# Kernel optimization log

Measured on AMD Instinct MI355X. Metric: run time of the kernel, lower is better.

## Reference

```python
import jax, jax.numpy as jnp
import numpy as np

# 27 kernel taps x 3 offset components (dz, dy, dx), matching the module's offset0 list.
OFFSET0 = np.array([
    1, 1, 1, 1, 1, 0, 1, 1, -1, 1, 0, 1, 1, 0, 0, 1, 0, -1, 1, -1, 1, 1, -1, 0, 1, -1, -1,
    0, 1, 1, 0, 1, 0, 0, 1, -1, 0, 0, 1, 0, 0, 0, 0, 0, -1, 0, -1, 1, 0, -1, 0, 0, -1, -1,
    -1, 1, 1, -1, 1, 0, -1, 1, -1, -1, 0, 1, -1, 0, 0, -1, 0, -1, -1, -1, 1, -1, -1, 0, -1, -1, -1
], dtype=np.float64).reshape(27, 3)

BN_EPS = 1e-5


def upsample_nearest2(x):
    # nn.Upsample(scale_factor=2), default mode='nearest', on [B,C,Z,Y,X]
    x = jnp.repeat(x, 2, axis=2)
    x = jnp.repeat(x, 2, axis=3)
    return jnp.repeat(x, 2, axis=4)


def deform_conv3d_static(x, W, b, alpha):
    """3D deformable conv, kernel 3, pad 1, stride 1, with spatially-constant
    per-tap offsets alpha*OFFSET0. Zero padding outside; trilinear sampling.
    Since offsets are static, each tap samples at a fixed fractional shift,
    implemented as a static trilinear combination of slices of the padded input.
    x: [B,C,Z,Y,X], W: [O,C,3,3,3], b: [O].
    """
    B, C, Z, Y, X = x.shape
    # pad 2: 1 for the 3x3x3 kernel + 1 for fractional offsets (|alpha*d| <= 0.7)
    xp = jnp.pad(x, ((0, 0), (0, 0), (2, 2), (2, 2), (2, 2)))
    out = None
    t = 0
    for kz in range(3):
        for ky in range(3):
            for kx in range(3):
                dz, dy, dx = (alpha * OFFSET0[t]).tolist()
                s = (kz - 1 + dz, ky - 1 + dy, kx - 1 + dx)  # shift rel. to output voxel
                f = [int(np.floor(v)) for v in s]
                w = [v - fl for v, fl in zip(s, f)]
                vol = None
                for cz in (0, 1):
                    for cy in (0, 1):
                        for cx in (0, 1):
                            wt = ((w[0] if cz else 1.0 - w[0]) *
                                  (w[1] if cy else 1.0 - w[1]) *
                                  (w[2] if cx else 1.0 - w[2]))
                            if wt == 0.0:
                                continue
                            z0 = 2 + f[0] + cz
                            y0 = 2 + f[1] + cy
                            x0 = 2 + f[2] + cx
                            sl = xp[:, :, z0:z0 + Z, y0:y0 + Y, x0:x0 + X]
                            sl = jnp.float32(wt) * sl
                            vol = sl if vol is None else vol + sl
                contrib = jnp.einsum('oc,bczyx->bozyx', W[:, :, kz, ky, kx], vol)
                out = contrib if out is None else out + contrib
                t += 1
    return out + b[None, :, None, None, None]


def batchnorm(x, g, bt, m, v):
    # eval-mode BatchNorm3d over channel axis 1
    inv = g * jax.lax.rsqrt(v + BN_EPS)
    return x * inv[None, :, None, None, None] + (bt - m * inv)[None, :, None, None, None]


def setup_inputs() -> dict:
    key = jax.random.key(0)
    ks = jax.random.split(key, 13)
    ch_in, ch_out = 64, 32
    x = jax.random.normal(ks[0], (1, ch_in, 32, 32, 32), jnp.float32)
    w_def = jax.random.normal(ks[1], (ch_out, ch_in, 3, 3, 3), jnp.float32) * 0.05
    b_def = jax.random.normal(ks[2], (ch_out,), jnp.float32) * 0.05
    bn1_g = 1.0 + 0.1 * jax.random.normal(ks[3], (ch_out,), jnp.float32)
    bn1_b = 0.1 * jax.random.normal(ks[4], (ch_out,), jnp.float32)
    bn1_m = 0.1 * jax.random.normal(ks[5], (ch_out,), jnp.float32)
    bn1_v = jax.random.uniform(ks[6], (ch_out,), jnp.float32, 0.5, 1.5)
    w_comb = jax.random.normal(ks[7], (ch_out, 3 * ch_out), jnp.float32) * 0.1
    b_comb = 0.05 * jax.random.normal(ks[8], (ch_out,), jnp.float32)
    bn2_g = 1.0 + 0.1 * jax.random.normal(ks[9], (ch_out,), jnp.float32)
    bn2_b = 0.1 * jax.random.normal(ks[10], (ch_out,), jnp.float32)
    bn2_m = 0.1 * jax.random.normal(ks[11], (ch_out,), jnp.float32)
    bn2_v = jax.random.uniform(ks[12], (ch_out,), jnp.float32, 0.5, 1.5)
    return {"x": x, "w_def": w_def, "b_def": b_def,
            "bn1_g": bn1_g, "bn1_b": bn1_b, "bn1_m": bn1_m, "bn1_v": bn1_v,
            "w_comb": w_comb, "b_comb": b_comb,
            "bn2_g": bn2_g, "bn2_b": bn2_b, "bn2_m": bn2_m, "bn2_v": bn2_v}


def reference(x, w_def, b_def, bn1_g, bn1_b, bn1_m, bn1_v,
              w_comb, b_comb, bn2_g, bn2_b, bn2_m, bn2_v):
    xu = upsample_nearest2(x)
    branches = []
    for alpha in (0.0, 0.4, 0.7):  # shared deform-conv weights, three static offset scales
        o = deform_conv3d_static(xu, w_def, b_def, alpha)
        o = jax.nn.relu(batchnorm(o, bn1_g, bn1_b, bn1_m, bn1_v))
        branches.append(o)
    cat = jnp.concatenate(branches, axis=1)  # [B, 3*ch_out, Z,Y,X]
    y = jnp.einsum('oc,bczyx->bozyx', w_comb, cat) + b_comb[None, :, None, None, None]
    y = batchnorm(y, bn2_g, bn2_b, bn2_m, bn2_v)
    return jax.nn.relu(y)
```

## Files before the change

kernel.cpp:

```cpp
#include <hip/hip_runtime.h>


typedef __bf16 bf16x8 __attribute__((ext_vector_type(8)));
typedef float f32x16 __attribute__((ext_vector_type(16)));
typedef unsigned u32x2 __attribute__((ext_vector_type(2)));

__device__ inline unsigned short f2bf(float f) {
  unsigned int u = __float_as_uint(f);
  u += 0x7FFFu + ((u >> 16) & 1u);
  return (unsigned short)(u >> 16);
}

__device__ inline bf16x8 bc16(uint4 v) { return __builtin_bit_cast(bf16x8, v); }

__device__ inline unsigned cvtpk(float lo, float hi) {
  unsigned r;
  asm("v_cvt_pk_bf16_f32 %0, %1, %2" : "=v"(r) : "v"(lo), "v"(hi));
  return r;
}

__device__ inline void plswap(unsigned& a, unsigned& b) {
  u32x2 r = __builtin_amdgcn_permlane32_swap(a, b, false, false);
  a = r.x;
  b = r.y;
}

__device__ inline void gload16(const unsigned short* g, unsigned short* l) {
  __builtin_amdgcn_global_load_lds(
      (const __attribute__((address_space(1))) unsigned int*)(const void*)g,
      (__attribute__((address_space(3))) unsigned int*)(void*)l, 16, 0, 0);
}

__device__ inline float ucoef(int abit, int k, int jbit, float alpha) {
  if (abit == 0) return (k == 0) ? (jbit ? alpha : 1.f - alpha) : (jbit ? 1.f : 0.f);
  return (k == 2) ? (jbit ? 1.f - alpha : alpha) : (jbit ? 0.f : 1.f);
}

__global__ void k_prep(const float* __restrict__ x, unsigned short* __restrict__ xT,
                       const float* __restrict__ w_def, const float* __restrict__ bn1_g,
                       const float* __restrict__ bn1_v, unsigned short* __restrict__ W_sw,
                       const float* __restrict__ w_comb, const float* __restrict__ b_comb,
                       const float* __restrict__ bn2_g, const float* __restrict__ bn2_b,
                       const float* __restrict__ bn2_m, const float* __restrict__ bn2_v,
                       const float* __restrict__ b_def, const float* __restrict__ bn1_b,
                       const float* __restrict__ bn1_m, unsigned short* __restrict__ W2_sw,
                       float* __restrict__ bias1, float* __restrict__ bias2) {
  __shared__ unsigned short t[64][65];
  int bid = blockIdx.x;
  if (bid < 512) {
    int s0 = bid * 64;
    int lane = threadIdx.x & 63;
    int grp = threadIdx.x >> 6;
#pragma unroll
    for (int c = grp; c < 64; c += 4)
      t[c][lane] = f2bf(x[c * 32768 + s0 + lane]);
    __syncthreads();
#pragma unroll
    for (int s = grp; s < 64; s += 4)
      xT[(size_t)(s0 + s) * 64 + lane] = t[lane][s];
  } else if (bid < 2048) {
    int e = (bid - 512) * 256 + threadIdx.x;
    int j = e & 7;
    int lane = (e >> 3) & 63;
    int idx = e >> 9;
    int nt = idx % 3;
    idx /= 3;
    int s = idx & 31;
    int p = idx >> 5;
    int o = lane & 31;
    int br = nt;
    int kk = 16 * s + ((lane >> 5) << 3) + j;
    int tap = kk >> 6, ch = kk & 63;
    int jz = (tap >> 2) & 1, jy = (tap >> 1) & 1, jx = tap & 1;
    int a = (p >> 2) & 1, b = (p >> 1) & 1, cp = p & 1;
    float alpha = (br == 0) ? 0.f : ((br == 1) ? 0.4f : 0.7f);
    const float* wb = w_def + (o * 64 + ch) * 27;
    float sum = 0.f;
    for (int kz = 0; kz < 3; ++kz) {
      float uz = ucoef(a, kz, jz, alpha);
      if (uz == 0.f) continue;
      for (int ky = 0; ky < 3; ++ky) {
        float uy = ucoef(b, ky, jy, alpha);
        if (uy == 0.f) continue;
        float uzy = uz * uy;
        for (int kx = 0; kx < 3; ++kx) {
          float ux = ucoef(cp, kx, jx, alpha);
          if (ux != 0.f) sum += wb[kz * 9 + ky * 3 + kx] * uzy * ux;
        }
      }
    }
    float s1 = bn1_g[o] * rsqrtf(bn1_v[o] + 1e-5f);
    W_sw[e] = f2bf(sum * s1);
  } else {
    int tid = threadIdx.x;
    for (int e = tid; e < 3072; e += 256) {
      int j = e & 7;
      int lane = (e >> 3) & 63;
      int s2 = e >> 9;
      int n = lane & 31;
      int k = 16 * s2 + ((lane >> 5) << 3) + j;
      float sc2 = bn2_g[n] * rsqrtf(bn2_v[n] + 1e-5f);
      W2_sw[e] = f2bf(w_comb[n * 96 + k] * sc2);
    }
    if (tid < 32) {
      float s1 = bn1_g[tid] * rsqrtf(bn1_v[tid] + 1e-5f);
      bias1[tid] = (b_def[tid] - bn1_m[tid]) * s1 + bn1_b[tid];
      float s2 = bn2_g[tid] * rsqrtf(bn2_v[tid] + 1e-5f);
      bias2[tid] = (b_comb[tid] - bn2_m[tid]) * s2 + bn2_b[tid];
    }
  }
}

__launch_bounds__(512, 2)
__global__ void k_main(const unsigned short* __restrict__ xT,
                       const unsigned short* __restrict__ W_sw,
                       const unsigned short* __restrict__ W2_sw,
                       const float* __restrict__ bias1f,
                       const float* __restrict__ bias2f,
                       float* __restrict__ out) {
  __shared__ unsigned short xt[51840];
  __shared__ unsigned short wring[2][6144];
  __shared__ float blds[64];
  int tid = threadIdx.x;
  int lane = tid & 63;
  int wv = tid >> 6;
  int bid = blockIdx.x;
  int bph = bid & 1, a = (bid >> 1) & 1;
  int tb = bid >> 2;
  int tx = tb & 3, ty = (tb >> 2) & 3, tz = tb >> 4;
  int i0 = tz * 8, j0 = ty * 8, k0 = tx * 8;

  for (int t2 = tid; t2 < 6480; t2 += 512) {
    int cblk = t2 & 7;
    int r = t2 >> 3;
    int xrel = r % 10;
    int zy = r / 10;
    int yrel = zy % 9;
    int zrel = zy / 9;
    int gz = i0 + a - 1 + zrel, gy = j0 + bph - 1 + yrel, gx = k0 - 1 + xrel;
    uint4 v = make_uint4(0u, 0u, 0u, 0u);
    if ((unsigned)gz < 32u && (unsigned)gy < 32u && (unsigned)gx < 32u)
      v = *(const uint4*)(xT + ((((gz * 32 + gy) * 32 + gx) << 6) + (cblk << 3)));
    *(uint4*)(xt + ((r << 6) + (((cblk + r) << 3) & 63))) = v;
  }
  if (tid < 32) {
    blds[tid] = bias1f[tid];
    blds[32 + tid] = bias2f[tid];
  }

  bf16x8 b2f[6];
  const uint4* w2q = (const uint4*)W2_sw;
#pragma unroll
  for (int s2 = 0; s2 < 6; ++s2) b2f[s2] = bc16(w2q[s2 * 64 + lane]);
  __syncthreads();

  int h = lane >> 5, h8 = h << 3;
  int m = lane & 31;
  int ax = m & 7, ay = (m >> 3) & 1, az = m >> 4;
  int zs = wv >> 2, ys = wv & 3;
  int dz0 = 4 * zs + az;
  int dy = 2 * ys + ay;
  int p0 = (a << 2) | (bph << 1);

  auto stage = [&](int pn, int tn, int slot) {
    if (wv < 6) {
      const unsigned short* g =
          W_sw + (size_t)pn * 49152 + tn * 6144 + wv * 1024 + lane * 8;
      unsigned short* l = &wring[slot][wv * 1024];
      gload16(g, l);
      gload16(g + 512, l + 512);
    }
  };

  stage(p0, 0, 0);

  volatile const float* vbl = blds;
  f32x16 osv0, osv1;

#pragma unroll
  for (int cp = 0; cp < 2; ++cp) {
    f32x16 acc[2][3];
#pragma unroll
    for (int mt = 0; mt < 2; ++mt)
#pragma unroll
      for (int nt = 0; nt < 3; ++nt) acc[mt][nt] = (f32x16)0.f;

#pragma unroll
    for (int t = 0; t < 8; ++t) {
      int c = cp * 8 + t;
      asm volatile("s_waitcnt vmcnt(0)" ::: "memory");
      __builtin_amdgcn_s_barrier();
      __builtin_amdgcn_sched_barrier(0);
      if (c < 15) {
        int cn = c + 1;
        stage(p0 | (cn >> 3), cn & 7, cn & 1);
      }
      __builtin_amdgcn_sched_barrier(0);
      const unsigned short* wb = &wring[c & 1][0];
      int jz = (t >> 2) & 1, jy = (t >> 1) & 1, jx = t & 1;
      int row0 = ((dz0 + jz) * 9 + (dy + jy)) * 10 + (ax + cp + jx);
      int row1 = row0 + 180;
      __builtin_amdgcn_s_setprio(1);
#pragma unroll
      for (int q = 0; q < 4; ++q) {
        int c0 = (q << 4) + h8;
        int e0 = (row0 << 6) + ((c0 + (row0 << 3)) & 63);
        int e1 = (row1 << 6) + ((c0 + (row1 << 3)) & 63);
        bf16x8 a0 = bc16(*(const uint4*)(xt + e0));
        bf16x8 a1 = bc16(*(const uint4*)(xt + e1));
        const unsigned short* wf = wb + q * 1536 + lane * 8;
        bf16x8 bb0 = bc16(*(const uint4*)(wf));
        bf16x8 bb1 = bc16(*(const uint4*)(wf + 512));
        bf16x8 bb2 = bc16(*(const uint4*)(wf + 1024));
        acc[0][0] = __builtin_amdgcn_mfma_f32_32x32x16_bf16(bb0, a0, acc[0][0], 0, 0, 0);
        acc[1][0] = __builtin_amdgcn_mfma_f32_32x32x16_bf16(bb0, a1, acc[1][0], 0, 0, 0);
        acc[0][1] = __builtin_amdgcn_mfma_f32_32x32x16_bf16(bb1, a0, acc[0][1], 0, 0, 0);
        acc[1][1] = __builtin_amdgcn_mfma_f32_32x32x16_bf16(bb1, a1, acc[1][1], 0, 0, 0);
        acc[0][2] = __builtin_amdgcn_mfma_f32_32x32x16_bf16(bb2, a0, acc[0][2], 0, 0, 0);
        acc[1][2] = __builtin_amdgcn_mfma_f32_32x32x16_bf16(bb2, a1, acc[1][2], 0, 0, 0);
      }
      __builtin_amdgcn_s_setprio(0);
      __builtin_amdgcn_sched_barrier(0);
    }

#pragma unroll
    for (int mt = 0; mt < 2; ++mt) {
      uint4 fr[6];
#pragma unroll
      for (int nt = 0; nt < 3; ++nt) {
        unsigned ww[8];
#pragma unroll
        for (int qc = 0; qc < 8; ++qc) {
          int q = qc >> 1, c2 = qc & 1;
          int r0 = 4 * q + 2 * c2;
          int row = (r0 & 3) + ((r0 >> 2) << 3) + (h << 2);
          float lo = fmaxf(acc[mt][nt][r0] + vbl[row], 0.f);
          float hi = fmaxf(acc[mt][nt][r0 + 1] + vbl[row + 1], 0.f);
          ww[2 * q + c2] = cvtpk(lo, hi);
        }
        plswap(ww[0], ww[2]);
        plswap(ww[1], ww[3]);
        plswap(ww[4], ww[6]);
        plswap(ww[5], ww[7]);
        fr[2 * nt] = make_uint4(ww[0], ww[1], ww[2], ww[3]);
        fr[2 * nt + 1] = make_uint4(ww[4], ww[5], ww[6], ww[7]);
      }
      f32x16 acc2 = (f32x16)0.f;
#pragma unroll
      for (int s2 = 0; s2 < 6; ++s2)
        acc2 = __builtin_amdgcn_mfma_f32_32x32x16_bf16(b2f[s2], bc16(fr[s2]), acc2, 0, 0, 0);
      if (cp == 0) {
        f32x16 ov;
#pragma unroll
        for (int r = 0; r < 16; ++r) {
          int row = (r & 3) + ((r >> 2) << 3) + (h << 2);
          ov[r] = fmaxf(acc2[r] + vbl[32 + row], 0.f);
        }
        if (mt == 0) osv0 = ov; else osv1 = ov;
      } else {
        f32x16 prev = (mt == 0) ? osv0 : osv1;
        int Z = 2 * (i0 + 4 * zs + 2 * mt + az) + a;
        int Y = 2 * (j0 + dy) + bph;
        float2* o2 = (float2*)out;
#pragma unroll
        for (int r = 0; r < 16; ++r) {
          int ch = (r & 3) + ((r >> 2) << 3) + (h << 2);
          float v1 = fmaxf(acc2[r] + vbl[32 + ch], 0.f);
          o2[((size_t)ch << 17) + ((size_t)Z << 11) + (Y << 5) + (k0 + ax)] =
              make_float2(prev[r], v1);
        }
      }
    }
  }
}

extern "C" void kernel_launch(void* const* d_in, const int* in_sizes, int n_in,
                              void* d_out, int out_size, void* d_ws, size_t ws_size,
                              hipStream_t stream) {
  (void)in_sizes; (void)n_in; (void)out_size; (void)ws_size;
  const float* x      = (const float*)d_in[0];
  const float* w_def  = (const float*)d_in[1];
  const float* b_def  = (const float*)d_in[2];
  const float* bn1_g  = (const float*)d_in[3];
  const float* bn1_b  = (const float*)d_in[4];
  const float* bn1_m  = (const float*)d_in[5];
  const float* bn1_v  = (const float*)d_in[6];
  const float* w_comb = (const float*)d_in[7];
  const float* b_comb = (const float*)d_in[8];
  const float* bn2_g  = (const float*)d_in[9];
  const float* bn2_b  = (const float*)d_in[10];
  const float* bn2_m  = (const float*)d_in[11];
  const float* bn2_v  = (const float*)d_in[12];

  char* ws = (char*)d_ws;
  unsigned short* xT   = (unsigned short*)(ws);
  unsigned short* W_sw = (unsigned short*)(ws + 4194304);
  unsigned short* W2sw = (unsigned short*)(ws + 4980736);
  float* bias1 = (float*)(ws + 4986880);
  float* bias2 = (float*)(ws + 4987008);
  float* out = (float*)d_out;

  hipLaunchKernelGGL(k_prep, dim3(2049), dim3(256), 0, stream,
                     x, xT, w_def, bn1_g, bn1_v, W_sw,
                     w_comb, b_comb, bn2_g, bn2_b, bn2_m, bn2_v,
                     b_def, bn1_b, bn1_m, W2sw, bias1, bias2);
  hipLaunchKernelGGL(k_main, dim3(256), dim3(512), 0, stream,
                     xT, W_sw, W2sw, bias1, bias2, out);
}
```

Measured before the change: 62.77 us.

## Stage two weight taps per barrier and stagger per-wave quarter order

The weight ring slots double in size so each stage loads two taps (12288 elements) using all eight waves instead of six. That halves the number of barrier/wait stages from 16 to 8. Each wave now starts its inner loop at a different quarter offset (qr), which spreads LDS bank accesses across waves. The loop over stages is no longer fully unrolled, the epilogue for the first half runs conditionally inside the loop, and the volatile bias reads become plain LDS reads. The costs are more LDS per block, which could threaten two blocks per CU, and different code generation for the partly rolled loop.

Result: faster. 52.91 us (-15.7%).

```diff
diff --git a/kernel.cpp b/kernel.cpp
--- a/kernel.cpp
+++ b/kernel.cpp
@@ -119,7 +119,7 @@
                        const float* __restrict__ bias2f,
                        float* __restrict__ out) {
   __shared__ unsigned short xt[51840];
-  __shared__ unsigned short wring[2][6144];
+  __shared__ unsigned short wring[2][12288];
   __shared__ float blds[64];
   int tid = threadIdx.x;
   int lane = tid & 63;
@@ -162,114 +162,139 @@
   int dy = 2 * ys + ay;
   int p0 = (a << 2) | (bph << 1);
 
-  auto stage = [&](int pn, int tn, int slot) {
-    if (wv < 6) {
-      const unsigned short* g =
-          W_sw + (size_t)pn * 49152 + tn * 6144 + wv * 1024 + lane * 8;
-      unsigned short* l = &wring[slot][wv * 1024];
-      gload16(g, l);
-      gload16(g + 512, l + 512);
-    }
+  auto stage = [&](int cc) {
+    int pn = p0 | (cc >> 2);
+    const unsigned short* g =
+        W_sw + (size_t)pn * 49152 + (cc & 3) * 12288 + wv * 1536 + lane * 8;
+    unsigned short* l = &wring[cc & 1][wv * 1536];
+    gload16(g, l);
+    gload16(g + 512, l + 512);
+    gload16(g + 1024, l + 1024);
   };
 
-  stage(p0, 0, 0);
-
-  volatile const float* vbl = blds;
+  stage(0);
+
   f32x16 osv0, osv1;
-
-#pragma unroll
-  for (int cp = 0; cp < 2; ++cp) {
-    f32x16 acc[2][3];
-#pragma unroll
-    for (int mt = 0; mt < 2; ++mt)
-#pragma unroll
-      for (int nt = 0; nt < 3; ++nt) acc[mt][nt] = (f32x16)0.f;
-
-#pragma unroll
-    for (int t = 0; t < 8; ++t) {
-      int c = cp * 8 + t;
-      asm volatile("s_waitcnt vmcnt(0)" ::: "memory");
-      __builtin_amdgcn_s_barrier();
-      __builtin_amdgcn_sched_barrier(0);
-      if (c < 15) {
-        int cn = c + 1;
-        stage(p0 | (cn >> 3), cn & 7, cn & 1);
-      }
-      __builtin_amdgcn_sched_barrier(0);
-      const unsigned short* wb = &wring[c & 1][0];
-      int jz = (t >> 2) & 1, jy = (t >> 1) & 1, jx = t & 1;
+  f32x16 acc[2][3];
+#pragma unroll
+  for (int mt = 0; mt < 2; ++mt)
+#pragma unroll
+    for (int nt = 0; nt < 3; ++nt) acc[mt][nt] = (f32x16)0.f;
+
+  int qr = (wv & 3) * 2;
+
+  for (int cc = 0; cc < 8; ++cc) {
+    asm volatile("s_waitcnt vmcnt(0)" ::: "memory");
+    __builtin_amdgcn_s_barrier();
+    __builtin_amdgcn_sched_barrier(0);
+    if (cc < 7) stage(cc + 1);
+    __builtin_amdgcn_sched_barrier(0);
+    int cp = cc >> 2;
+    int tb2 = (cc & 3) * 2;
+    const unsigned short* wfb = &wring[cc & 1][lane * 8];
+#pragma unroll
+    for (int i = 0; i < 8; ++i) {
+      int q2 = (i + qr) & 7;
+      int tl = q2 >> 2, q = q2 & 3;
+      int t8 = tb2 + tl;
+      int jz = (t8 >> 2) & 1, jy = (t8 >> 1) & 1, jx = t8 & 1;
       int row0 = ((dz0 + jz) * 9 + (dy + jy)) * 10 + (ax + cp + jx);
       int row1 = row0 + 180;
+      int c0 = (q << 4) + h8;
+      int e0 = (row0 << 6) + ((c0 + (row0 << 3)) & 63);
+      int e1 = (row1 << 6) + ((c0 + (row1 << 3)) & 63);
+      bf16x8 a0 = bc16(*(const uint4*)(xt + e0));
+      bf16x8 a1 = bc16(*(const uint4*)(xt + e1));
+      const unsigned short* wf = wfb + tl * 6144 + q * 1536;
+      bf16x8 bb0 = bc16(*(const uint4*)(wf));
+      bf16x8 bb1 = bc16(*(const uint4*)(wf + 512));
+      bf16x8 bb2 = bc16(*(const uint4*)(wf + 1024));
       __builtin_amdgcn_s_setprio(1);
-#pragma unroll
-      for (int q = 0; q < 4; ++q) {
-        int c0 = (q << 4) + h8;
-        int e0 = (row0 << 6) + ((c0 + (row0 << 3)) & 63);
-        int e1 = (row1 << 6) + ((c0 + (row1 << 3)) & 63);
-        bf16x8 a0 = bc16(*(const uint4*)(xt + e0));
-        bf16x8 a1 = bc16(*(const uint4*)(xt + e1));
-        const unsigned short* wf = wb + q * 1536 + lane * 8;
-        bf16x8 bb0 = bc16(*(const uint4*)(wf));
-        bf16x8 bb1 = bc16(*(const uint4*)(wf + 512));
-        bf16x8 bb2 = bc16(*(const uint4*)(wf + 1024));
-        acc[0][0] = __builtin_amdgcn_mfma_f32_32x32x16_bf16(bb0, a0, acc[0][0], 0, 0, 0);
-        acc[1][0] = __builtin_amdgcn_mfma_f32_32x32x16_bf16(bb0, a1, acc[1][0], 0, 0, 0);
-        acc[0][1] = __builtin_amdgcn_mfma_f32_32x32x16_bf16(bb1, a0, acc[0][1], 0, 0, 0);
-        acc[1][1] = __builtin_amdgcn_mfma_f32_32x32x16_bf16(bb1, a1, acc[1][1], 0, 0, 0);
-        acc[0][2] = __builtin_amdgcn_mfma_f32_32x32x16_bf16(bb2, a0, acc[0][2], 0, 0, 0);
-        acc[1][2] = __builtin_amdgcn_mfma_f32_32x32x16_bf16(bb2, a1, acc[1][2], 0, 0, 0);
-      }
+      acc[0][0] = __builtin_amdgcn_mfma_f32_32x32x16_bf16(bb0, a0, acc[0][0], 0, 0, 0);
+      acc[1][0] = __builtin_amdgcn_mfma_f32_32x32x16_bf16(bb0, a1, acc[1][0], 0, 0, 0);
+      acc[0][1] = __builtin_amdgcn_mfma_f32_32x32x16_bf16(bb1, a0, acc[0][1], 0, 0, 0);
+      acc[1][1] = __builtin_amdgcn_mfma_f32_32x32x16_bf16(bb1, a1, acc[1][1], 0, 0, 0);
+      acc[0][2] = __builtin_amdgcn_mfma_f32_32x32x16_bf16(bb2, a0, acc[0][2], 0, 0, 0);
+      acc[1][2] = __builtin_amdgcn_mfma_f32_32x32x16_bf16(bb2, a1, acc[1][2], 0, 0, 0);
       __builtin_amdgcn_s_setprio(0);
-      __builtin_amdgcn_sched_barrier(0);
-    }
-
-#pragma unroll
-    for (int mt = 0; mt < 2; ++mt) {
-      uint4 fr[6];
-#pragma unroll
-      for (int nt = 0; nt < 3; ++nt) {
-        unsigned ww[8];
-#pragma unroll
-        for (int qc = 0; qc < 8; ++qc) {
-          int q = qc >> 1, c2 = qc & 1;
-          int r0 = 4 * q + 2 * c2;
-          int row = (r0 & 3) + ((r0 >> 2) << 3) + (h << 2);
-          float lo = fmaxf(acc[mt][nt][r0] + vbl[row], 0.f);
-          float hi = fmaxf(acc[mt][nt][r0 + 1] + vbl[row + 1], 0.f);
-          ww[2 * q + c2] = cvtpk(lo, hi);
+    }
+
+    if (cc == 3) {
+#pragma unroll
+      for (int mt = 0; mt < 2; ++mt) {
+        uint4 fr[6];
+#pragma unroll
+        for (int nt = 0; nt < 3; ++nt) {
+          unsigned ww[8];
+#pragma unroll
+          for (int qc = 0; qc < 8; ++qc) {
+            int q = qc >> 1, c2 = qc & 1;
+            int r0 = 4 * q + 2 * c2;
+            int row = (r0 & 3) + ((r0 >> 2) << 3) + (h << 2);
+            float lo = fmaxf(acc[mt][nt][r0] + blds[row], 0.f);
+            float hi = fmaxf(acc[mt][nt][r0 + 1] + blds[row + 1], 0.f);
+            ww[2 * q + c2] = cvtpk(lo, hi);
+          }
+          plswap(ww[0], ww[2]);
+          plswap(ww[1], ww[3]);
+          plswap(ww[4], ww[6]);
+          plswap(ww[5], ww[7]);
+          fr[2 * nt] = make_uint4(ww[0], ww[1], ww[2], ww[3]);
+          fr[2 * nt + 1] = make_uint4(ww[4], ww[5], ww[6], ww[7]);
         }
-        plswap(ww[0], ww[2]);
-        plswap(ww[1], ww[3]);
-        plswap(ww[4], ww[6]);
-        plswap(ww[5], ww[7]);
-        fr[2 * nt] = make_uint4(ww[0], ww[1], ww[2], ww[3]);
-        fr[2 * nt + 1] = make_uint4(ww[4], ww[5], ww[6], ww[7]);
-      }
-      f32x16 acc2 = (f32x16)0.f;
-#pragma unroll
-      for (int s2 = 0; s2 < 6; ++s2)
-        acc2 = __builtin_amdgcn_mfma_f32_32x32x16_bf16(b2f[s2], bc16(fr[s2]), acc2, 0, 0, 0);
-      if (cp == 0) {
+        f32x16 acc2 = (f32x16)0.f;
+#pragma unroll
+        for (int s2 = 0; s2 < 6; ++s2)
+          acc2 = __builtin_amdgcn_mfma_f32_32x32x16_bf16(b2f[s2], bc16(fr[s2]), acc2, 0, 0, 0);
         f32x16 ov;
 #pragma unroll
         for (int r = 0; r < 16; ++r) {
           int row = (r & 3) + ((r >> 2) << 3) + (h << 2);
-          ov[r] = fmaxf(acc2[r] + vbl[32 + row], 0.f);
+          ov[r] = fmaxf(acc2[r] + blds[32 + row], 0.f);
         }
         if (mt == 0) osv0 = ov; else osv1 = ov;
-      } else {
-        f32x16 prev = (mt == 0) ? osv0 : osv1;
-        int Z = 2 * (i0 + 4 * zs + 2 * mt + az) + a;
-        int Y = 2 * (j0 + dy) + bph;
-        float2* o2 = (float2*)out;
-#pragma unroll
-        for (int r = 0; r < 16; ++r) {
-          int ch = (r & 3) + ((r >> 2) << 3) + (h << 2);
-          float v1 = fmaxf(acc2[r] + vbl[32 + ch], 0.f);
-          o2[((size_t)ch << 17) + ((size_t)Z << 11) + (Y << 5) + (k0 + ax)] =
-              make_float2(prev[r], v1);
-        }
+#pragma unroll
+        for (int nt = 0; nt < 3; ++nt) acc[mt][nt] = (f32x16)0.f;
       }
+    }
+  }
+
+#pragma unroll
+  for (int mt = 0; mt < 2; ++mt) {
+    uint4 fr[6];
+#pragma unroll
+    for (int nt = 0; nt < 3; ++nt) {
+      unsigned ww[8];
+#pragma unroll
+      for (int qc = 0; qc < 8; ++qc) {
+        int q = qc >> 1, c2 = qc & 1;
+        int r0 = 4 * q + 2 * c2;
+        int row = (r0 & 3) + ((r0 >> 2) << 3) + (h << 2);
+        float lo = fmaxf(acc[mt][nt][r0] + blds[row], 0.f);
+        float hi = fmaxf(acc[mt][nt][r0 + 1] + blds[row + 1], 0.f);
+        ww[2 * q + c2] = cvtpk(lo, hi);
+      }
+      plswap(ww[0], ww[2]);
+      plswap(ww[1], ww[3]);
+      plswap(ww[4], ww[6]);
+      plswap(ww[5], ww[7]);
+      fr[2 * nt] = make_uint4(ww[0], ww[1], ww[2], ww[3]);
+      fr[2 * nt + 1] = make_uint4(ww[4], ww[5], ww[6], ww[7]);
+    }
+    f32x16 acc2 = (f32x16)0.f;
+#pragma unroll
+    for (int s2 = 0; s2 < 6; ++s2)
+      acc2 = __builtin_amdgcn_mfma_f32_32x32x16_bf16(b2f[s2], bc16(fr[s2]), acc2, 0, 0, 0);
+    f32x16 prev = (mt == 0) ? osv0 : osv1;
+    int Z = 2 * (i0 + 4 * zs + 2 * mt + az) + a;
+    int Y = 2 * (j0 + dy) + bph;
+    float2* o2 = (float2*)out;
+#pragma unroll
+    for (int r = 0; r < 16; ++r) {
+      int ch = (r & 3) + ((r >> 2) << 3) + (h << 2);
+      float v1 = fmaxf(acc2[r] + blds[32 + ch], 0.f);
+      o2[((size_t)ch << 17) + ((size_t)Z << 11) + (Y << 5) + (k0 + ax)] =
+          make_float2(prev[r], v1);
     }
   }
 }
```
